# Performance work log

Measured on AMD Instinct MI355X. Metric: run time of the kernel, lower is better.

Reference implementation:

```python
import jax, jax.numpy as jnp
import numpy as np

NUM_HEADS = 12
EMBED_DIM = 768


def setup_inputs() -> dict:
    key = jax.random.key(0)
    ks = jax.random.split(key, 7)
    B, N, E = 4, 2048, EMBED_DIM
    s = 1.0 / np.sqrt(E)  # init scale to keep activations sane
    return {
        "x": jax.random.normal(ks[0], (B, N, E), dtype=jnp.float32),
        "Wq": jax.random.normal(ks[1], (E, E), dtype=jnp.float32) * s,
        "bq": jnp.zeros((E,), dtype=jnp.float32),
        "Wk": jax.random.normal(ks[2], (E, E), dtype=jnp.float32) * s,
        "bk": jnp.zeros((E,), dtype=jnp.float32),
        "Wv": jax.random.normal(ks[3], (E, E), dtype=jnp.float32) * s,
        "bv": jnp.zeros((E,), dtype=jnp.float32),
    }


def reference(x, Wq, bq, Wk, bk, Wv, bv):
    B, N, E = x.shape
    H = NUM_HEADS
    d = E // H
    # QKV projections, split into heads: b n (h d) -> b h n d
    q = (x @ Wq + bq).reshape(B, N, H, d).transpose(0, 2, 1, 3)
    k = (x @ Wk + bk).reshape(B, N, H, d).transpose(0, 2, 1, 3)
    v = (x @ Wv + bv).reshape(B, N, H, d).transpose(0, 2, 1, 3)
    # NOTE: non-standard scale = 1/sqrt(num_heads), not 1/sqrt(head_dim)
    scale = 1.0 / jnp.sqrt(jnp.asarray(H, dtype=x.dtype))
    attn_weight = jnp.einsum("bhqd,bhkd->bhqk", q, k) * scale
    # NOTE: softmax over the QUERY axis (dim=2), not the key axis
    attn_score = jax.nn.softmax(attn_weight, axis=2)
    out = jnp.einsum("bhqk,bhkd->bhqd", attn_score, v)
    # b h n d -> b n (h d)
    return out.transpose(0, 2, 1, 3).reshape(B, N, E)
```

## Files before the change

kernel.cpp:

```cpp
#include <hip/hip_runtime.h>

#define NN 2048
#define EE 768
#define HH 12
#define DD 64
#define BHX 48
#define MM 8192

typedef unsigned short u16;
typedef unsigned int u32;
typedef __attribute__((ext_vector_type(8))) short bf16x8;
typedef __attribute__((ext_vector_type(4))) float f32x4;

#if __has_builtin(__builtin_amdgcn_exp2f)
#define EX2(x) __builtin_amdgcn_exp2f(x)
#else
#define EX2(x) exp2f(x)
#endif

#define MFMA16(a, b, c) __builtin_amdgcn_mfma_f32_16x16x32_bf16((a), (b), (c), 0, 0, 0)

__device__ __forceinline__ u16 f2bf(float f) {
    u32 u = __builtin_bit_cast(u32, f);
    u32 r = (u + 0x7FFFu + ((u >> 16) & 1u)) >> 16;
    return (u16)r;
}
__device__ __forceinline__ float bf2f(u16 b) {
    u32 u = ((u32)b) << 16;
    return __builtin_bit_cast(float, u);
}
__device__ __forceinline__ void gload_lds16(const u16* g, u16* l) {
    __builtin_amdgcn_global_load_lds((const __attribute__((address_space(1))) void*)g,
                                     (__attribute__((address_space(3))) void*)l, 16, 0, 0);
}

__global__ __launch_bounds__(256) void k_cvt_x(const float* __restrict__ x, u16* __restrict__ xb, int n8) {
    int i = blockIdx.x * 256 + threadIdx.x;
    if (i >= n8) return;
    const float4* x4 = (const float4*)x;
    float4 a = x4[i * 2], b = x4[i * 2 + 1];
    uint4 o;
    o.x = (u32)f2bf(a.x) | ((u32)f2bf(a.y) << 16);
    o.y = (u32)f2bf(a.z) | ((u32)f2bf(a.w) << 16);
    o.z = (u32)f2bf(b.x) | ((u32)f2bf(b.y) << 16);
    o.w = (u32)f2bf(b.z) | ((u32)f2bf(b.w) << 16);
    ((uint4*)xb)[i] = o;
}

__global__ __launch_bounds__(256) void k_wt(const float* __restrict__ Wq, const float* __restrict__ Wk,
                                            const float* __restrict__ Wv, u16* __restrict__ wt) {
    __shared__ u16 lt[64 * 80];
    const int z = blockIdx.z;
    const float* W = (z == 0) ? Wq : (z == 1 ? Wk : Wv);
    const int k0 = blockIdx.x * 64, j0 = blockIdx.y * 64;
    const int tid = threadIdx.x;
#pragma unroll
    for (int p = 0; p < 4; ++p) {
        int c = p * 256 + tid;
        int kk = c >> 4, j4 = (c & 15) * 4;
        float4 v = *(const float4*)(W + (size_t)(k0 + kk) * EE + j0 + j4);
        lt[(j4 + 0) * 80 + kk] = f2bf(v.x);
        lt[(j4 + 1) * 80 + kk] = f2bf(v.y);
        lt[(j4 + 2) * 80 + kk] = f2bf(v.z);
        lt[(j4 + 3) * 80 + kk] = f2bf(v.w);
    }
    __syncthreads();
    u16* dstz = wt + (size_t)z * EE * EE;
#pragma unroll
    for (int p = 0; p < 2; ++p) {
        int c = p * 256 + tid;
        int j = c >> 3, kc = c & 7;
        uint4 o = *(const uint4*)&lt[j * 80 + kc * 8];
        *(uint4*)(dstz + (size_t)(j0 + j) * EE + k0 + kc * 8) = o;
    }
}

__global__ __launch_bounds__(256) void k_proj(const u16* __restrict__ xb, const u16* __restrict__ wt,
                                              const float* __restrict__ bq, const float* __restrict__ bk,
                                              const float* __restrict__ bv, u16* __restrict__ qh,
                                              u16* __restrict__ kh, u16* __restrict__ vh) {
    __shared__ u16 lA[128 * 32];
    __shared__ u16 lB[128 * 32];
    const int z = blockIdx.z;
    const u16* Wz = wt + (size_t)z * EE * EE;
    const float* bias = (z == 0) ? bq : (z == 1 ? bk : bv);
    u16* outp = (z == 0) ? qh : (z == 1 ? kh : vh);
    const float oscale = (z == 0) ? (0.28867513459481287f * 1.4426950408889634f) : 1.0f;
    const int tid = threadIdx.x;
    const int lane = tid & 63, w = tid >> 6;
    const int wr = w >> 1, wc = w & 1, lr = lane & 15, lg = lane >> 4;
    const int m0 = blockIdx.x * 128, n0 = blockIdx.y * 128;

    f32x4 acc[4][4];
#pragma unroll
    for (int mi = 0; mi < 4; mi++)
#pragma unroll
        for (int ni = 0; ni < 4; ni++) acc[mi][ni] = (f32x4){0.f, 0.f, 0.f, 0.f};

    for (int kt = 0; kt < EE; kt += 32) {
#pragma unroll
        for (int i = 0; i < 2; i++) {
            int c = i * 256 + tid;
            int row = c >> 2, cc = c & 3;
            gload_lds16(xb + (size_t)(m0 + row) * EE + kt + cc * 8, &lA[c * 8]);
            gload_lds16(Wz + (size_t)(n0 + row) * EE + kt + cc * 8, &lB[c * 8]);
        }
        __syncthreads();
        bf16x8 af[4], bfr[4];
#pragma unroll
        for (int mi = 0; mi < 4; mi++) af[mi] = *(const bf16x8*)&lA[(wr * 64 + mi * 16 + lr) * 32 + lg * 8];
#pragma unroll
        for (int ni = 0; ni < 4; ni++) bfr[ni] = *(const bf16x8*)&lB[(wc * 64 + ni * 16 + lr) * 32 + lg * 8];
#pragma unroll
        for (int mi = 0; mi < 4; mi++)
#pragma unroll
            for (int ni = 0; ni < 4; ni++) acc[mi][ni] = MFMA16(af[mi], bfr[ni], acc[mi][ni]);
        __syncthreads();
    }

#pragma unroll
    for (int ni = 0; ni < 4; ni++) {
        int col = n0 + wc * 64 + ni * 16 + lr;
        float bb = bias[col];
        int h = col >> 6, dd = col & 63;
#pragma unroll
        for (int mi = 0; mi < 4; mi++) {
            int rowbase = m0 + wr * 64 + mi * 16 + lg * 4;
#pragma unroll
            for (int r = 0; r < 4; r++) {
                int row = rowbase + r;
                int b = row >> 11, nn = row & 2047;
                outp[(((size_t)b * HH + h) * NN + nn) * DD + dd] = f2bf((acc[mi][ni][r] + bb) * oscale);
            }
        }
    }
}

__global__ __launch_bounds__(512) void k_stats(const u16* __restrict__ qh, const u16* __restrict__ kh,
                                               float* __restrict__ rlb) {
    __shared__ u16 lds[2][4096];
    const int lin = blockIdx.x;
    const int nb = (lin & 7) * 96 + (lin >> 3);
    const int bh = nb >> 4, kb = nb & 15;
    const int tid = threadIdx.x, lane = tid & 63, w = tid >> 6;
    const int lr = lane & 15, lg = lane >> 4;
    const int kw0 = kb * 128 + w * 16;
    const u16* Q = qh + (size_t)bh * NN * DD;
    const u16* K = kh + (size_t)bh * NN * DD;

    bf16x8 kf[2];
#pragma unroll
    for (int kk = 0; kk < 2; kk++)
        kf[kk] = *(const bf16x8*)(K + (size_t)(kw0 + lr) * DD + kk * 32 + lg * 8);

    const int c = tid;
    const int f = c >> 6;
    const int qrow = (f >> 1) * 16 + (c & 15);
    const int doff = (f & 1) * 32 + ((c >> 4) & 3) * 8;
    const u16* qp = Q + (size_t)qrow * DD + doff;

#define STAGE_Q(buf, q0) gload_lds16(qp + (size_t)(q0) * DD, &lds[buf][c * 8])

    STAGE_Q(0, 0);
    __syncthreads();
    float lacc = 0.f;
    int cur = 0;
    for (int it = 0; it < 32; ++it) {
        if (it < 31) STAGE_Q(cur ^ 1, (it + 1) * 64);
#pragma unroll
        for (int qt = 0; qt < 4; ++qt) {
            bf16x8 qa0 = *(const bf16x8*)&lds[cur][(qt * 2 + 0) * 512 + lane * 8];
            bf16x8 qa1 = *(const bf16x8*)&lds[cur][(qt * 2 + 1) * 512 + lane * 8];
            f32x4 ss = (f32x4){0.f, 0.f, 0.f, 0.f};
            ss = MFMA16(qa0, kf[0], ss);
            ss = MFMA16(qa1, kf[1], ss);
            lacc += EX2(ss[0]) + EX2(ss[1]) + EX2(ss[2]) + EX2(ss[3]);
        }
        __syncthreads();
        cur ^= 1;
    }
#undef STAGE_Q
    float v = lacc;
    v += __shfl_xor(v, 16);
    v += __shfl_xor(v, 32);
    if (lane < 16) rlb[(size_t)bh * NN + kw0 + lane] = 1.0f / v;
}

__global__ __launch_bounds__(256) void k_vtrans(const u16* __restrict__ vh, const float* __restrict__ rlb,
                                                u16* __restrict__ vt) {
    __shared__ u16 lds[64 * 80];
    const int bh = blockIdx.x, n0 = blockIdx.y * 64;
    const int tid = threadIdx.x;
    const u16* src = vh + (size_t)bh * NN * DD + (size_t)n0 * DD;
    const float* rlp = rlb + (size_t)bh * NN + n0;
#pragma unroll
    for (int i = 0; i < 2; i++) {
        int c = i * 256 + tid;
        int row = c >> 3, dc = c & 7;
        uint4 vraw = *(const uint4*)(src + row * DD + dc * 8);
        float rk = rlp[row];
        u32 uu[4] = {vraw.x, vraw.y, vraw.z, vraw.w};
#pragma unroll
        for (int j = 0; j < 4; j++) {
            u16 e0 = (u16)(uu[j] & 0xffff), e1 = (u16)(uu[j] >> 16);
            lds[(dc * 8 + 2 * j) * 80 + row] = f2bf(rk * bf2f(e0));
            lds[(dc * 8 + 2 * j + 1) * 80 + row] = f2bf(rk * bf2f(e1));
        }
    }
    __syncthreads();
    u16* dst = vt + (size_t)bh * DD * NN + n0;
#pragma unroll
    for (int i = 0; i < 2; i++) {
        int c = i * 256 + tid;
        int d = c >> 3, nc = c & 7;
        int w0 = nc * 8;
        uint2 a = *(const uint2*)&lds[d * 80 + w0];
        uint2 b = *(const uint2*)&lds[d * 80 + w0 + 4];
        int hi32 = (w0 >> 5) * 32;
        int wa = w0 & 31, wb = (w0 + 4) & 31;
        int ca = ((wa & 15) >> 2) * 8 + (wa >> 4) * 4;
        int cb = ((wb & 15) >> 2) * 8 + (wb >> 4) * 4;
        *(uint2*)(dst + (size_t)d * NN + hi32 + ca) = a;
        *(uint2*)(dst + (size_t)d * NN + hi32 + cb) = b;
    }
}

__global__ __launch_bounds__(512) void k_attn(const u16* __restrict__ qh, const u16* __restrict__ kh,
                                              const u16* __restrict__ vt, float* __restrict__ out) {
    __shared__ u16 lds[2][8192];
    const int lin = blockIdx.x;
    const int nb = (lin & 7) * 96 + (lin >> 3);
    const int bh = nb >> 4, qb = nb & 15;
    const int tid = threadIdx.x, lane = tid & 63, w = tid >> 6;
    const int lr = lane & 15, lg = lane >> 4;
    const int qw0 = qb * 128 + w * 16;
    const u16* Q = qh + (size_t)bh * NN * DD;
    const u16* K = kh + (size_t)bh * NN * DD;
    const u16* V = vt + (size_t)bh * DD * NN;

    bf16x8 qf[2];
#pragma unroll
    for (int kk = 0; kk < 2; kk++)
        qf[kk] = *(const bf16x8*)(Q + (size_t)(qw0 + lr) * DD + kk * 32 + lg * 8);

    const int c = tid;
    const int f = c >> 6;
    const int rk = (f >> 2) * 32 + ((f >> 1) & 1) * 16 + (c & 15);
    const int doff = (f & 1) * 32 + ((c >> 4) & 3) * 8;
    const u16* kp = K + (size_t)rk * DD + doff;
    const int drow = (f & 3) * 16 + (c & 15);
    const int koff = (f >> 2) * 32 + ((c >> 4) & 3) * 8;
    const u16* vp = V + (size_t)drow * NN + koff;

#define STAGE_KV(buf, k0)                                          \
    do {                                                           \
        gload_lds16(kp + (size_t)(k0) * DD, &lds[buf][c * 8]);     \
        gload_lds16(vp + (size_t)(k0), &lds[buf][4096 + c * 8]);   \
    } while (0)

    f32x4 acc[4];
#pragma unroll
    for (int di = 0; di < 4; di++) acc[di] = (f32x4){0.f, 0.f, 0.f, 0.f};

    STAGE_KV(0, 0);
    __syncthreads();
    int cur = 0;
    for (int it = 0; it < 32; ++it) {
        if (it < 31) STAGE_KV(cur ^ 1, (it + 1) * 64);
        const u16* Lk = &lds[cur][0];
        const u16* Lv = &lds[cur][4096];
#pragma unroll
        for (int kc = 0; kc < 2; ++kc) {
            bf16x8 kf2[2][2];
#pragma unroll
            for (int t = 0; t < 2; t++)
#pragma unroll
                for (int kk = 0; kk < 2; kk++)
                    kf2[t][kk] = *(const bf16x8*)&Lk[((kc * 2 + t) * 2 + kk) * 512 + lane * 8];
            bf16x8 vf[4];
#pragma unroll
            for (int di = 0; di < 4; di++)
                vf[di] = *(const bf16x8*)&Lv[(kc * 4 + di) * 512 + lane * 8];
            f32x4 s0 = (f32x4){0.f, 0.f, 0.f, 0.f}, s1 = (f32x4){0.f, 0.f, 0.f, 0.f};
            s0 = MFMA16(kf2[0][0], qf[0], s0);
            s0 = MFMA16(kf2[0][1], qf[1], s0);
            s1 = MFMA16(kf2[1][0], qf[0], s1);
            s1 = MFMA16(kf2[1][1], qf[1], s1);
            uint4 pu;
            pu.x = (u32)f2bf(EX2(s0[0])) | ((u32)f2bf(EX2(s0[1])) << 16);
            pu.y = (u32)f2bf(EX2(s0[2])) | ((u32)f2bf(EX2(s0[3])) << 16);
            pu.z = (u32)f2bf(EX2(s1[0])) | ((u32)f2bf(EX2(s1[1])) << 16);
            pu.w = (u32)f2bf(EX2(s1[2])) | ((u32)f2bf(EX2(s1[3])) << 16);
            bf16x8 pa = __builtin_bit_cast(bf16x8, pu);
#pragma unroll
            for (int di = 0; di < 4; di++) acc[di] = MFMA16(pa, vf[di], acc[di]);
        }
        __syncthreads();
        cur ^= 1;
    }
#undef STAGE_KV

    const int b = bh / HH, h = bh % HH;
#pragma unroll
    for (int di = 0; di < 4; di++)
#pragma unroll
        for (int r = 0; r < 4; r++) {
            int q = qw0 + lg * 4 + r;
            int d = di * 16 + lr;
            out[((size_t)(b * NN + q)) * EE + h * DD + d] = acc[di][r];
        }
}

extern "C" void kernel_launch(void* const* d_in, const int* in_sizes, int n_in,
                              void* d_out, int out_size, void* d_ws, size_t ws_size,
                              hipStream_t stream) {
    const float* x = (const float*)d_in[0];
    const float* Wq = (const float*)d_in[1];
    const float* bq = (const float*)d_in[2];
    const float* Wk = (const float*)d_in[3];
    const float* bk = (const float*)d_in[4];
    const float* Wv = (const float*)d_in[5];
    const float* bv = (const float*)d_in[6];
    float* out = (float*)d_out;
    char* ws = (char*)d_ws;

    size_t off = 0;
    u16* xb = (u16*)(ws + off); off += (size_t)MM * EE * 2;
    u16* wt = (u16*)(ws + off); off += (size_t)3 * EE * EE * 2;
    u16* qh = (u16*)(ws + off); off += (size_t)BHX * NN * DD * 2;
    u16* kh = (u16*)(ws + off); off += (size_t)BHX * NN * DD * 2;
    u16* vh = (u16*)(ws + off); off += (size_t)BHX * NN * DD * 2;
    u16* vt = (u16*)(ws + off); off += (size_t)BHX * NN * DD * 2;
    float* rlb = (float*)(ws + off); off += (size_t)BHX * NN * 4;

    k_cvt_x<<<dim3(3072), dim3(256), 0, stream>>>(x, xb, MM * EE / 8);
    k_wt<<<dim3(12, 12, 3), dim3(256), 0, stream>>>(Wq, Wk, Wv, wt);
    k_proj<<<dim3(64, 6, 3), dim3(256), 0, stream>>>(xb, wt, bq, bk, bv, qh, kh, vh);
    k_stats<<<dim3(768), dim3(512), 0, stream>>>(qh, kh, rlb);
    k_vtrans<<<dim3(48, 32), dim3(256), 0, stream>>>(vh, rlb, vt);
    k_attn<<<dim3(768), dim3(512), 0, stream>>>(qh, kh, vt, out);
}
```

Baseline: 173.4 us.

## Split key range across wave groups with 32-row query tiles per wave

The attention kernel now gives each wave 32 query rows instead of 16, so every K/V fragment loaded from LDS feeds two MFMA chains. The 8 waves form two groups that each process half of the key sequence, so the main loop runs 16 iterations, staging both halves into a doubled LDS buffer. At the end the two groups' partial accumulators are summed through LDS before the store. The aim is fewer LDS reads per MFMA and fewer loop iterations and barriers, at the cost of more registers, double the LDS footprint (64KB), which may cut occupancy, and an extra reduction step.

```diff
diff --git a/kernel.cpp b/kernel.cpp
--- a/kernel.cpp
+++ b/kernel.cpp
@@ -227,21 +227,24 @@
 
 __global__ __launch_bounds__(512) void k_attn(const u16* __restrict__ qh, const u16* __restrict__ kh,
                                               const u16* __restrict__ vt, float* __restrict__ out) {
-    __shared__ u16 lds[2][8192];
+    __shared__ u16 lds[2][16384];
     const int lin = blockIdx.x;
     const int nb = (lin & 7) * 96 + (lin >> 3);
     const int bh = nb >> 4, qb = nb & 15;
     const int tid = threadIdx.x, lane = tid & 63, w = tid >> 6;
     const int lr = lane & 15, lg = lane >> 4;
-    const int qw0 = qb * 128 + w * 16;
+    const int g = w >> 2;
+    const int qw0 = qb * 128 + (w & 3) * 32;
     const u16* Q = qh + (size_t)bh * NN * DD;
     const u16* K = kh + (size_t)bh * NN * DD;
     const u16* V = vt + (size_t)bh * DD * NN;
 
-    bf16x8 qf[2];
-#pragma unroll
-    for (int kk = 0; kk < 2; kk++)
-        qf[kk] = *(const bf16x8*)(Q + (size_t)(qw0 + lr) * DD + kk * 32 + lg * 8);
+    bf16x8 qf[2][2];
+#pragma unroll
+    for (int mi = 0; mi < 2; mi++)
+#pragma unroll
+        for (int kk = 0; kk < 2; kk++)
+            qf[mi][kk] = *(const bf16x8*)(Q + (size_t)(qw0 + mi * 16 + lr) * DD + kk * 32 + lg * 8);
 
     const int c = tid;
     const int f = c >> 6;
@@ -252,23 +255,27 @@
     const int koff = (f >> 2) * 32 + ((c >> 4) & 3) * 8;
     const u16* vp = V + (size_t)drow * NN + koff;
 
-#define STAGE_KV(buf, k0)                                          \
-    do {                                                           \
-        gload_lds16(kp + (size_t)(k0) * DD, &lds[buf][c * 8]);     \
-        gload_lds16(vp + (size_t)(k0), &lds[buf][4096 + c * 8]);   \
+#define STAGE_KV(buf, k0)                                                            \
+    do {                                                                             \
+        gload_lds16(kp + (size_t)(k0) * DD, &lds[buf][c * 8]);                       \
+        gload_lds16(vp + (size_t)(k0), &lds[buf][4096 + c * 8]);                     \
+        gload_lds16(kp + (size_t)((k0) + 1024) * DD, &lds[buf][8192 + c * 8]);       \
+        gload_lds16(vp + (size_t)(k0) + 1024, &lds[buf][12288 + c * 8]);             \
     } while (0)
 
-    f32x4 acc[4];
-#pragma unroll
-    for (int di = 0; di < 4; di++) acc[di] = (f32x4){0.f, 0.f, 0.f, 0.f};
+    f32x4 acc[2][4];
+#pragma unroll
+    for (int mi = 0; mi < 2; mi++)
+#pragma unroll
+        for (int di = 0; di < 4; di++) acc[mi][di] = (f32x4){0.f, 0.f, 0.f, 0.f};
 
     STAGE_KV(0, 0);
     __syncthreads();
     int cur = 0;
-    for (int it = 0; it < 32; ++it) {
-        if (it < 31) STAGE_KV(cur ^ 1, (it + 1) * 64);
-        const u16* Lk = &lds[cur][0];
-        const u16* Lv = &lds[cur][4096];
+    for (int it = 0; it < 16; ++it) {
+        if (it < 15) STAGE_KV(cur ^ 1, (it + 1) * 64);
+        const u16* Lk = &lds[cur][g * 8192];
+        const u16* Lv = &lds[cur][g * 8192 + 4096];
 #pragma unroll
         for (int kc = 0; kc < 2; ++kc) {
             bf16x8 kf2[2][2];
@@ -281,34 +288,53 @@
 #pragma unroll
             for (int di = 0; di < 4; di++)
                 vf[di] = *(const bf16x8*)&Lv[(kc * 4 + di) * 512 + lane * 8];
-            f32x4 s0 = (f32x4){0.f, 0.f, 0.f, 0.f}, s1 = (f32x4){0.f, 0.f, 0.f, 0.f};
-            s0 = MFMA16(kf2[0][0], qf[0], s0);
-            s0 = MFMA16(kf2[0][1], qf[1], s0);
-            s1 = MFMA16(kf2[1][0], qf[0], s1);
-            s1 = MFMA16(kf2[1][1], qf[1], s1);
-            uint4 pu;
-            pu.x = (u32)f2bf(EX2(s0[0])) | ((u32)f2bf(EX2(s0[1])) << 16);
-            pu.y = (u32)f2bf(EX2(s0[2])) | ((u32)f2bf(EX2(s0[3])) << 16);
-            pu.z = (u32)f2bf(EX2(s1[0])) | ((u32)f2bf(EX2(s1[1])) << 16);
-            pu.w = (u32)f2bf(EX2(s1[2])) | ((u32)f2bf(EX2(s1[3])) << 16);
-            bf16x8 pa = __builtin_bit_cast(bf16x8, pu);
-#pragma unroll
-            for (int di = 0; di < 4; di++) acc[di] = MFMA16(pa, vf[di], acc[di]);
+#pragma unroll
+            for (int mi = 0; mi < 2; mi++) {
+                f32x4 s0 = (f32x4){0.f, 0.f, 0.f, 0.f}, s1 = (f32x4){0.f, 0.f, 0.f, 0.f};
+                s0 = MFMA16(kf2[0][0], qf[mi][0], s0);
+                s0 = MFMA16(kf2[0][1], qf[mi][1], s0);
+                s1 = MFMA16(kf2[1][0], qf[mi][0], s1);
+                s1 = MFMA16(kf2[1][1], qf[mi][1], s1);
+                uint4 pu;
+                pu.x = (u32)f2bf(EX2(s0[0])) | ((u32)f2bf(EX2(s0[1])) << 16);
+                pu.y = (u32)f2bf(EX2(s0[2])) | ((u32)f2bf(EX2(s0[3])) << 16);
+                pu.z = (u32)f2bf(EX2(s1[0])) | ((u32)f2bf(EX2(s1[1])) << 16);
+                pu.w = (u32)f2bf(EX2(s1[2])) | ((u32)f2bf(EX2(s1[3])) << 16);
+                bf16x8 pa = __builtin_bit_cast(bf16x8, pu);
+#pragma unroll
+                for (int di = 0; di < 4; di++) acc[mi][di] = MFMA16(pa, vf[di], acc[mi][di]);
+            }
         }
         __syncthreads();
         cur ^= 1;
     }
 #undef STAGE_KV
 
-    const int b = bh / HH, h = bh % HH;
-#pragma unroll
-    for (int di = 0; di < 4; di++)
-#pragma unroll
-        for (int r = 0; r < 4; r++) {
-            int q = qw0 + lg * 4 + r;
-            int d = di * 16 + lr;
-            out[((size_t)(b * NN + q)) * EE + h * DD + d] = acc[di][r];
-        }
+    f32x4* fb4 = (f32x4*)&lds[0][0];
+    if (w >= 4) {
+#pragma unroll
+        for (int mi = 0; mi < 2; mi++)
+#pragma unroll
+            for (int di = 0; di < 4; di++)
+                fb4[(mi * 4 + di) * 256 + (w - 4) * 64 + lane] = acc[mi][di];
+    }
+    __syncthreads();
+    if (w < 4) {
+        const int b = bh / HH, h = bh % HH;
+#pragma unroll
+        for (int mi = 0; mi < 2; mi++)
+#pragma unroll
+            for (int di = 0; di < 4; di++) {
+                f32x4 o = fb4[(mi * 4 + di) * 256 + w * 64 + lane];
+                acc[mi][di] += o;
+#pragma unroll
+                for (int r = 0; r < 4; r++) {
+                    int q = qw0 + mi * 16 + lg * 4 + r;
+                    int d = di * 16 + lr;
+                    out[((size_t)(b * NN + q)) * EE + h * DD + d] = acc[mi][di][r];
+                }
+            }
+    }
 }
 
 extern "C" void kernel_launch(void* const* d_in, const int* in_sizes, int n_in,
```

Measured after the change: 174.6 us. No clear change (+0.7%).
